# Kernel tuning notes

Hardware: AMD Instinct MI355X
Metric: run time of the kernel (lower is better)

The kernel has to match this reference:

```python
import jax, jax.numpy as jnp
import numpy as np

N_NODES = 500_000
N_EDGES = 16_000_000
F_IN, F_HID, F_OUT = 5, 5, 8


def _gcn_conv(x, W, b, src, dst, norm, n):
    # x: [N, Fin] -> transform first (cheaper than transforming messages)
    h = x @ W                              # [N, Fout]
    msg = h[src] * norm[:, None]           # [E', Fout] gather + per-edge scale
    out = jax.ops.segment_sum(msg, dst, num_segments=n)  # scatter-add over dst
    return out + b


def setup_inputs() -> dict:
    key = jax.random.key(0)
    ks = jax.random.split(key, 6)
    x = jax.random.normal(ks[0], (N_NODES, F_IN), dtype=jnp.float32)
    edge_index = jax.random.randint(ks[1], (2, N_EDGES), 0, N_NODES, dtype=jnp.int32)
    # Glorot-ish init for the two GCNConv layers
    W1 = jax.random.normal(ks[2], (F_IN, F_HID), dtype=jnp.float32) / np.sqrt(F_IN)
    b1 = jnp.zeros((F_HID,), dtype=jnp.float32)
    W2 = jax.random.normal(ks[3], (F_HID, F_OUT), dtype=jnp.float32) / np.sqrt(F_HID)
    b2 = jnp.zeros((F_OUT,), dtype=jnp.float32)
    return {"x": x, "edge_index": edge_index, "W1": W1, "b1": b1, "W2": W2, "b2": b2}


def reference(x, edge_index, W1, b1, W2, b2):
    n = x.shape[0]
    # GCNConv default: add self-loops, symmetric D^-1/2 A D^-1/2 normalization
    loops = jnp.arange(n, dtype=edge_index.dtype)
    src = jnp.concatenate([edge_index[0], loops])
    dst = jnp.concatenate([edge_index[1], loops])
    deg = jax.ops.segment_sum(jnp.ones_like(dst, dtype=x.dtype), dst, num_segments=n)
    dinv = jnp.where(deg > 0, jax.lax.rsqrt(deg), 0.0)
    norm = dinv[src] * dinv[dst]           # [E + N]

    h = _gcn_conv(x, W1, b1, src, dst, norm, n)
    h = jax.nn.relu(h)
    # F.dropout with training=False is the identity (eval-mode reference)
    h = _gcn_conv(h, W2, b2, src, dst, norm, n)
    return jax.nn.log_softmax(h, axis=1)
```

## Files before the change

kernel.cpp:

```cpp
#include <hip/hip_runtime.h>
#include <math.h>


#define FIN 5
#define FHID 5
#define FOUT 8
#define RB 256
#define EPA 24576
#define NBUCK_MAX 2048
#define OCAP 10240

typedef _Float16 half8 __attribute__((ext_vector_type(8)));
typedef int int4v __attribute__((ext_vector_type(4)));


__global__ void k_scan1(const int* __restrict__ t, int* __restrict__ scn,
                        int* __restrict__ partial, int n) {
    __shared__ int sh[256];
    int tx = threadIdx.x;
    int i = blockIdx.x * 256 + tx;
    int v = (i < n) ? t[i] : 0;
    sh[tx] = v;
    __syncthreads();
    for (int off = 1; off < 256; off <<= 1) {
        int add = (tx >= off) ? sh[tx - off] : 0;
        __syncthreads();
        sh[tx] += add;
        __syncthreads();
    }
    if (i < n) scn[i] = sh[tx] - v;
    if (tx == 255) partial[blockIdx.x] = sh[255];
}

__global__ void k_scan2(int* __restrict__ partial, int nb) {
    __shared__ int sh[256];
    __shared__ int carry;
    int tx = threadIdx.x;
    if (tx == 0) carry = 0;
    __syncthreads();
    for (int base = 0; base < nb; base += 256) {
        int i = base + tx;
        int v = (i < nb) ? partial[i] : 0;
        int c0 = carry;
        sh[tx] = v;
        __syncthreads();
        for (int off = 1; off < 256; off <<= 1) {
            int add = (tx >= off) ? sh[tx - off] : 0;
            __syncthreads();
            sh[tx] += add;
            __syncthreads();
        }
        if (i < nb) partial[i] = c0 + sh[tx] - v;
        __syncthreads();
        if (tx == 0) carry = c0 + sh[255];
        __syncthreads();
    }
}


__global__ void k_histA(const int* __restrict__ dst, int* __restrict__ cnt,
                        int e, int nbuck, int nblkA) {
    __shared__ int hist[NBUCK_MAX];
    int tx = threadIdx.x, blk = blockIdx.x;
    for (int b = tx; b < nbuck; b += 1024) hist[b] = 0;
    __syncthreads();
    size_t base = (size_t)blk * EPA;
    const int4v* dst4 = (const int4v*)dst;
    for (int k = 0; k < EPA / 4096; ++k) {
        size_t e4 = base / 4 + (size_t)k * 1024 + tx;
        size_t i = e4 * 4;
        if (i + 3 < (size_t)e) {
            int4v d4 = __builtin_nontemporal_load(&dst4[e4]);
#pragma unroll
            for (int j = 0; j < 4; ++j) atomicAdd(&hist[d4[j] >> 8], 1);
        } else {
            for (int j = 0; j < 4; ++j) {
                size_t ii = i + j;
                if (ii < (size_t)e) atomicAdd(&hist[dst[ii] >> 8], 1);
            }
        }
    }
    __syncthreads();
    for (int b = tx; b < nbuck; b += 1024) cnt[(size_t)b * nblkA + blk] = hist[b];
}

__global__ void k_scatterA(const int* __restrict__ src, const int* __restrict__ dst,
                           const int* __restrict__ scn, const int* __restrict__ part,
                           unsigned int* __restrict__ binnedA,
                           int e, int nbuck, int nblkA) {
    __shared__ int lstart[NBUCK_MAX];
    __shared__ int cur[NBUCK_MAX];
    __shared__ int gbase[NBUCK_MAX];
    __shared__ unsigned int staged[EPA];
    int tx = threadIdx.x, blk = blockIdx.x;
    for (int b = tx; b < NBUCK_MAX; b += 1024) lstart[b] = 0;
    for (int b = tx; b < nbuck; b += 1024) {
        size_t idx = (size_t)b * nblkA + blk;
        gbase[b] = scn[idx] + part[idx >> 8];
    }
    __syncthreads();
    size_t base = (size_t)blk * EPA;
    const int4v* dst4 = (const int4v*)dst;
    const int4v* src4 = (const int4v*)src;
    for (int k = 0; k < EPA / 4096; ++k) {
        size_t e4 = base / 4 + (size_t)k * 1024 + tx;
        size_t i = e4 * 4;
        if (i + 3 < (size_t)e) {
            int4v d4 = dst4[e4];
#pragma unroll
            for (int j = 0; j < 4; ++j) atomicAdd(&lstart[d4[j] >> 8], 1);
        } else {
            for (int j = 0; j < 4; ++j) {
                size_t ii = i + j;
                if (ii < (size_t)e) atomicAdd(&lstart[dst[ii] >> 8], 1);
            }
        }
    }
    __syncthreads();
    int j0 = tx, j1 = tx + 1024;
    int c0 = lstart[j0], c1 = lstart[j1];
    for (int off = 1; off < NBUCK_MAX; off <<= 1) {
        int a0 = (j0 >= off) ? lstart[j0 - off] : 0;
        int a1 = (j1 >= off) ? lstart[j1 - off] : 0;
        __syncthreads();
        lstart[j0] += a0; lstart[j1] += a1;
        __syncthreads();
    }
    int e0 = lstart[j0] - c0, e1 = lstart[j1] - c1;
    __syncthreads();
    lstart[j0] = e0; lstart[j1] = e1;
    cur[j0] = e0;    cur[j1] = e1;
    __syncthreads();
    for (int k = 0; k < EPA / 4096; ++k) {
        size_t e4 = base / 4 + (size_t)k * 1024 + tx;
        size_t i = e4 * 4;
        if (i + 3 < (size_t)e) {
            int4v d4 = dst4[e4];
            int4v s4 = src4[e4];
#pragma unroll
            for (int j = 0; j < 4; ++j) {
                int d = d4[j];
                int pos = atomicAdd(&cur[d >> 8], 1);
                staged[pos] = ((unsigned int)(d & (RB - 1)) << 19) | (unsigned int)s4[j];
            }
        } else {
            for (int j = 0; j < 4; ++j) {
                size_t ii = i + j;
                if (ii < (size_t)e) {
                    int d = dst[ii];
                    int pos = atomicAdd(&cur[d >> 8], 1);
                    staged[pos] = ((unsigned int)(d & (RB - 1)) << 19) | (unsigned int)src[ii];
                }
            }
        }
    }
    __syncthreads();
    int grp = tx >> 4, lane = tx & 15;
    for (int b = grp; b < nbuck; b += 64) {
        int ls = lstart[b];
        int le = (b + 1 < NBUCK_MAX) ? lstart[b + 1] : 0;
        int cnt = le - ls;
        int gb = gbase[b];
        for (int k = lane; k < cnt; k += 16)
            binnedA[gb + k] = staged[ls + k];
    }
}


__global__ void k_passC(const unsigned int* __restrict__ binnedA,
                        const int* __restrict__ scn, const int* __restrict__ part,
                        const float* __restrict__ x,
                        half8* __restrict__ g1, unsigned int* __restrict__ binned3,
                        int* __restrict__ nodeptr,
                        int n, int e, int nbuck, int nblkA) {
    __shared__ int hist[RB];
    __shared__ int scanbuf[RB];
    __shared__ int cur[RB];
    __shared__ unsigned int obuf[OCAP];
    int tx = threadIdx.x, b = blockIdx.x;
    if (tx < RB) hist[tx] = 0;
    __syncthreads();
    size_t i0 = (size_t)b * nblkA;
    int start = scn[i0] + part[i0 >> 8];
    int end;
    if (b + 1 < nbuck) {
        size_t i1 = (size_t)(b + 1) * nblkA;
        end = scn[i1] + part[i1 >> 8];
    } else {
        end = e;
    }
    int len = end - start;
    for (int i = start + tx; i < end; i += 512)
        atomicAdd(&hist[binnedA[i] >> 19], 1);
    __syncthreads();
    int v = 0;
    if (tx < RB) { v = hist[tx]; scanbuf[tx] = v; }
    __syncthreads();
    for (int off = 1; off < RB; off <<= 1) {
        int add = 0;
        if (tx < RB && tx >= off) add = scanbuf[tx - off];
        __syncthreads();
        if (tx < RB) scanbuf[tx] += add;
        __syncthreads();
    }
    if (tx < RB) {
        int excl = scanbuf[tx] - v;
        nodeptr[(size_t)b * RB + tx] = start + excl;
        cur[tx] = excl;
        int node = b * RB + tx;
        if (node < n) {
            float d = rsqrtf((float)(v + 1));
            const float* xp = x + (size_t)node * FIN;
            half8 row = {};
#pragma unroll
            for (int f = 0; f < FIN; ++f) row[f] = (_Float16)(xp[f] * d);
            row[5] = (_Float16)d;
            g1[node] = row;
        }
    }
    if (b == nbuck - 1 && tx == 0) nodeptr[(size_t)nbuck * RB] = end;
    __syncthreads();
    if (len <= OCAP) {
        for (int i = start + tx; i < end; i += 512) {
            unsigned int p = binnedA[i];
            int pos = atomicAdd(&cur[p >> 19], 1);
            obuf[pos] = p & 0x7FFFFu;
        }
        __syncthreads();
        for (int j = tx; j < len; j += 512)
            binned3[start + j] = obuf[j];
    } else {
        for (int i = start + tx; i < end; i += 512) {
            unsigned int p = binnedA[i];
            int pos = atomicAdd(&cur[p >> 19], 1);
            binned3[start + pos] = p & 0x7FFFFu;
        }
    }
}


__global__ void k_vagg1(const unsigned int* __restrict__ ed,
                        const int* __restrict__ nodeptr,
                        const half8* __restrict__ g1,
                        const float* __restrict__ W1, const float* __restrict__ b1,
                        half8* __restrict__ g2, int n) {
    int tid = blockIdx.x * blockDim.x + threadIdx.x;
    int node = tid >> 4;
    int lane = tid & 15;
    if (node >= n) return;
    int o0 = nodeptr[node];
    int o1 = nodeptr[node + 1];
    float a0 = 0, a1 = 0, a2 = 0, a3 = 0, a4 = 0;
    for (int k = o0 + lane; k < o1; k += 16) {
        unsigned int s = __builtin_nontemporal_load(&ed[k]);
        half8 hv = g1[s];
        a0 += (float)hv[0]; a1 += (float)hv[1]; a2 += (float)hv[2];
        a3 += (float)hv[3]; a4 += (float)hv[4];
    }
#pragma unroll
    for (int off = 1; off < 16; off <<= 1) {
        a0 += __shfl_xor(a0, off, 16);
        a1 += __shfl_xor(a1, off, 16);
        a2 += __shfl_xor(a2, off, 16);
        a3 += __shfl_xor(a3, off, 16);
        a4 += __shfl_xor(a4, off, 16);
    }
    if (lane == 0) {
        half8 gi = g1[node];
        float d = (float)gi[5];
        float v[FIN];
        v[0] = (a0 + (float)gi[0]) * d;
        v[1] = (a1 + (float)gi[1]) * d;
        v[2] = (a2 + (float)gi[2]) * d;
        v[3] = (a3 + (float)gi[3]) * d;
        v[4] = (a4 + (float)gi[4]) * d;
        half8 go = {};
#pragma unroll
        for (int j = 0; j < FHID; ++j) {
            float s = b1[j];
#pragma unroll
            for (int k = 0; k < FIN; ++k) s = fmaf(v[k], W1[k * FHID + j], s);
            go[j] = (_Float16)(fmaxf(s, 0.0f) * d);
        }
        go[5] = gi[5];
        g2[node] = go;
    }
}

__global__ void k_vagg2(const unsigned int* __restrict__ ed,
                        const int* __restrict__ nodeptr,
                        const half8* __restrict__ g2,
                        const float* __restrict__ W2, const float* __restrict__ b2,
                        float* __restrict__ out, int n) {
    int tid = blockIdx.x * blockDim.x + threadIdx.x;
    int node = tid >> 4;
    int lane = tid & 15;
    if (node >= n) return;
    int o0 = nodeptr[node];
    int o1 = nodeptr[node + 1];
    float a0 = 0, a1 = 0, a2 = 0, a3 = 0, a4 = 0;
    for (int k = o0 + lane; k < o1; k += 16) {
        unsigned int s = __builtin_nontemporal_load(&ed[k]);
        half8 hv = g2[s];
        a0 += (float)hv[0]; a1 += (float)hv[1]; a2 += (float)hv[2];
        a3 += (float)hv[3]; a4 += (float)hv[4];
    }
#pragma unroll
    for (int off = 1; off < 16; off <<= 1) {
        a0 += __shfl_xor(a0, off, 16);
        a1 += __shfl_xor(a1, off, 16);
        a2 += __shfl_xor(a2, off, 16);
        a3 += __shfl_xor(a3, off, 16);
        a4 += __shfl_xor(a4, off, 16);
    }
    if (lane == 0) {
        half8 gi = g2[node];
        float d = (float)gi[5];
        float v[FHID];
        v[0] = (a0 + (float)gi[0]) * d;
        v[1] = (a1 + (float)gi[1]) * d;
        v[2] = (a2 + (float)gi[2]) * d;
        v[3] = (a3 + (float)gi[3]) * d;
        v[4] = (a4 + (float)gi[4]) * d;
        float o[FOUT];
        float m = -1e30f;
#pragma unroll
        for (int j = 0; j < FOUT; ++j) {
            float s = b2[j];
#pragma unroll
            for (int k = 0; k < FHID; ++k) s = fmaf(v[k], W2[k * FOUT + j], s);
            o[j] = s;
            m = fmaxf(m, s);
        }
        float ssum = 0.0f;
#pragma unroll
        for (int j = 0; j < FOUT; ++j) ssum += expf(o[j] - m);
        float lse = m + logf(ssum);
        float* op = out + (size_t)node * FOUT;
#pragma unroll
        for (int j = 0; j < FOUT; ++j) op[j] = o[j] - lse;
    }
}


__global__ void f_init_deg(float* __restrict__ deg, int n) {
    int i = blockIdx.x * blockDim.x + threadIdx.x;
    if (i < n) deg[i] = 1.0f;
}
__global__ void f_count_deg(const int* __restrict__ dst, float* __restrict__ deg, int e) {
    int i = blockIdx.x * blockDim.x + threadIdx.x;
    if (i < e) atomicAdd(&deg[dst[i]], 1.0f);
}
__global__ void f_finish_deg_g1(const float* __restrict__ x, float* __restrict__ dinv,
                                float* __restrict__ g1, int n) {
    int i = blockIdx.x * blockDim.x + threadIdx.x;
    if (i >= n) return;
    float d = rsqrtf(dinv[i]);
    dinv[i] = d;
#pragma unroll
    for (int f = 0; f < FIN; ++f) g1[(size_t)i * FIN + f] = x[(size_t)i * FIN + f] * d;
}
__global__ void f_scatter5(const int* __restrict__ src, const int* __restrict__ dst,
                           const float* __restrict__ g, float* __restrict__ acc, int e) {
    int i = blockIdx.x * blockDim.x + threadIdx.x;
    if (i >= e) return;
    int s = src[i], d = dst[i];
    float* a = acc + (size_t)d * 5;
    const float* gp = g + (size_t)s * 5;
    atomicAdd(a + 0, gp[0]);
    atomicAdd(a + 1, gp[1]);
    atomicAdd(a + 2, gp[2]);
    atomicAdd(a + 3, gp[3]);
    atomicAdd(a + 4, gp[4]);
}
__global__ void f_update1(const float* __restrict__ dinv, float* __restrict__ g,
                          float* __restrict__ acc, const float* __restrict__ W1,
                          const float* __restrict__ b1, int n) {
    int i = blockIdx.x * blockDim.x + threadIdx.x;
    if (i >= n) return;
    float d = dinv[i];
    float v[FIN];
#pragma unroll
    for (int f = 0; f < FIN; ++f) {
        size_t idx = (size_t)i * FIN + f;
        v[f] = (acc[idx] + g[idx]) * d;
        acc[idx] = 0.0f;
    }
#pragma unroll
    for (int j = 0; j < FHID; ++j) {
        float s = b1[j];
#pragma unroll
        for (int k = 0; k < FIN; ++k) s += v[k] * W1[k * FHID + j];
        g[(size_t)i * FHID + j] = fmaxf(s, 0.0f) * d;
    }
}
__global__ void f_update2(const float* __restrict__ dinv, const float* __restrict__ g,
                          const float* __restrict__ acc, const float* __restrict__ W2,
                          const float* __restrict__ b2, float* __restrict__ out, int n) {
    int i = blockIdx.x * blockDim.x + threadIdx.x;
    if (i >= n) return;
    float d = dinv[i];
    float v[FHID];
#pragma unroll
    for (int f = 0; f < FHID; ++f) v[f] = (acc[(size_t)i * FHID + f] + g[(size_t)i * FHID + f]) * d;
    float o[FOUT];
    float m = -1e30f;
#pragma unroll
    for (int j = 0; j < FOUT; ++j) {
        float s = b2[j];
#pragma unroll
        for (int k = 0; k < FHID; ++k) s += v[k] * W2[k * FOUT + j];
        o[j] = s;
        m = fmaxf(m, s);
    }
    float ssum = 0.0f;
#pragma unroll
    for (int j = 0; j < FOUT; ++j) ssum += expf(o[j] - m);
    float lse = m + logf(ssum);
#pragma unroll
    for (int j = 0; j < FOUT; ++j) out[(size_t)i * FOUT + j] = o[j] - lse;
}


extern "C" void kernel_launch(void* const* d_in, const int* in_sizes, int n_in,
                              void* d_out, int out_size, void* d_ws, size_t ws_size,
                              hipStream_t stream) {
    const float* x  = (const float*)d_in[0];
    const int*   ei = (const int*)d_in[1];
    const float* W1 = (const float*)d_in[2];
    const float* b1 = (const float*)d_in[3];
    const float* W2 = (const float*)d_in[4];
    const float* b2 = (const float*)d_in[5];

    const int n = in_sizes[0] / FIN;
    const int e = in_sizes[1] / 2;
    const int* src = ei;
    const int* dst = ei + e;

    const int nbuck = (n + RB - 1) / RB;
    const int nblkA = (e + EPA - 1) / EPA;
    const size_t m = (size_t)nbuck * nblkA;
    const int nsb = (int)((m + 255) / 256);

    size_t off = 0;
    auto al = [&](size_t bytes) { size_t o = off; off = (off + bytes + 15) & ~(size_t)15; return o; };
    int*          cnt     = (int*)((char*)d_ws + al(m * 4));
    int*          scn     = (int*)((char*)d_ws + al(m * 4));
    int*          part    = (int*)((char*)d_ws + al((size_t)nsb * 4));
    int*          nptr    = (int*)((char*)d_ws + al(((size_t)nbuck * RB + 1) * 4));
    half8*        g1      = (half8*)((char*)d_ws + al((size_t)n * 16));
    unsigned int* binnedA = (unsigned int*)((char*)d_ws + al((size_t)e * 4));
    unsigned int* binned3 = (unsigned int*)((char*)d_ws + al((size_t)e * 4));
    half8*        g2      = (half8*)binnedA;
    const size_t need = off;

    if (ws_size >= need && n <= 524288 && n >= 1 && (e & 3) == 0 && nbuck <= NBUCK_MAX) {
        k_histA<<<nblkA, 1024, 0, stream>>>(dst, cnt, e, nbuck, nblkA);
        k_scan1<<<nsb, 256, 0, stream>>>(cnt, scn, part, (int)m);
        k_scan2<<<1, 256, 0, stream>>>(part, nsb);
        k_scatterA<<<nblkA, 1024, 0, stream>>>(src, dst, scn, part, binnedA, e, nbuck, nblkA);
        k_passC<<<nbuck, 512, 0, stream>>>(binnedA, scn, part, x, g1, binned3, nptr, n, e, nbuck, nblkA);
        const int ga = (int)(((size_t)n * 16 + 511) / 512);
        k_vagg1<<<ga, 512, 0, stream>>>(binned3, nptr, g1, W1, b1, g2, n);
        k_vagg2<<<ga, 512, 0, stream>>>(binned3, nptr, g2, W2, b2, (float*)d_out, n);
        return;
    }

    const int B = 256;
    const int gn = (n + B - 1) / B;
    const int ge = (e + B - 1) / B;
    float* fdinv = (float*)d_ws;
    float* fg    = fdinv + n;
    float* facc  = fg + (size_t)5 * n;
    hipMemsetAsync(facc, 0, (size_t)5 * n * sizeof(float), stream);
    f_init_deg<<<gn, B, 0, stream>>>(fdinv, n);
    f_count_deg<<<ge, B, 0, stream>>>(dst, fdinv, e);
    f_finish_deg_g1<<<gn, B, 0, stream>>>(x, fdinv, fg, n);
    f_scatter5<<<ge, B, 0, stream>>>(src, dst, fg, facc, e);
    f_update1<<<gn, B, 0, stream>>>(fdinv, fg, facc, W1, b1, n);
    f_scatter5<<<ge, B, 0, stream>>>(src, dst, fg, facc, e);
    f_update2<<<gn, B, 0, stream>>>(fdinv, fg, facc, W2, b2, (float*)d_out, n);
}
```

Measured before the change: 509.6 us.

## Split aggregation by source-node half to shrink gather working set

Each destination's edge list is now partitioned into sources below and above n/2, with a midptr array marking the split. Each layer's aggregation becomes two passes: the first gathers from the low half of the feature table into fp32 partial accumulators, and the second gathers from the high half and finishes the layer. The goal is to keep each pass's random-gather working set small enough to stay cache-resident, at the cost of extra kernel launches and partial-sum traffic. Separately, scatterA reuses the per-block histogram from histA instead of recomputing it, and reads src/dst with nontemporal loads.

```diff
diff --git a/kernel.cpp b/kernel.cpp
--- a/kernel.cpp
+++ b/kernel.cpp
@@ -12,6 +12,7 @@
 
 typedef _Float16 half8 __attribute__((ext_vector_type(8)));
 typedef int int4v __attribute__((ext_vector_type(4)));
+typedef float fl4 __attribute__((ext_vector_type(4)));
 
 
 __global__ void k_scan1(const int* __restrict__ t, int* __restrict__ scn,
@@ -85,6 +86,7 @@
 }
 
 __global__ void k_scatterA(const int* __restrict__ src, const int* __restrict__ dst,
+                           const int* __restrict__ cnt,
                            const int* __restrict__ scn, const int* __restrict__ part,
                            unsigned int* __restrict__ binnedA,
                            int e, int nbuck, int nblkA) {
@@ -93,11 +95,29 @@
     __shared__ int gbase[NBUCK_MAX];
     __shared__ unsigned int staged[EPA];
     int tx = threadIdx.x, blk = blockIdx.x;
-    for (int b = tx; b < NBUCK_MAX; b += 1024) lstart[b] = 0;
-    for (int b = tx; b < nbuck; b += 1024) {
-        size_t idx = (size_t)b * nblkA + blk;
-        gbase[b] = scn[idx] + part[idx >> 8];
-    }
+    for (int b = tx; b < NBUCK_MAX; b += 1024) {
+        if (b < nbuck) {
+            size_t idx = (size_t)b * nblkA + blk;
+            lstart[b] = cnt[idx];
+            gbase[b] = scn[idx] + part[idx >> 8];
+        } else {
+            lstart[b] = 0;
+        }
+    }
+    __syncthreads();
+    int j0 = tx, j1 = tx + 1024;
+    int c0 = lstart[j0], c1 = lstart[j1];
+    for (int off = 1; off < NBUCK_MAX; off <<= 1) {
+        int a0 = (j0 >= off) ? lstart[j0 - off] : 0;
+        int a1 = (j1 >= off) ? lstart[j1 - off] : 0;
+        __syncthreads();
+        lstart[j0] += a0; lstart[j1] += a1;
+        __syncthreads();
+    }
+    int e0 = lstart[j0] - c0, e1 = lstart[j1] - c1;
+    __syncthreads();
+    lstart[j0] = e0; lstart[j1] = e1;
+    cur[j0] = e0;    cur[j1] = e1;
     __syncthreads();
     size_t base = (size_t)blk * EPA;
     const int4v* dst4 = (const int4v*)dst;
@@ -106,37 +126,8 @@
         size_t e4 = base / 4 + (size_t)k * 1024 + tx;
         size_t i = e4 * 4;
         if (i + 3 < (size_t)e) {
-            int4v d4 = dst4[e4];
-#pragma unroll
-            for (int j = 0; j < 4; ++j) atomicAdd(&lstart[d4[j] >> 8], 1);
-        } else {
-            for (int j = 0; j < 4; ++j) {
-                size_t ii = i + j;
-                if (ii < (size_t)e) atomicAdd(&lstart[dst[ii] >> 8], 1);
-            }
-        }
-    }
-    __syncthreads();
-    int j0 = tx, j1 = tx + 1024;
-    int c0 = lstart[j0], c1 = lstart[j1];
-    for (int off = 1; off < NBUCK_MAX; off <<= 1) {
-        int a0 = (j0 >= off) ? lstart[j0 - off] : 0;
-        int a1 = (j1 >= off) ? lstart[j1 - off] : 0;
-        __syncthreads();
-        lstart[j0] += a0; lstart[j1] += a1;
-        __syncthreads();
-    }
-    int e0 = lstart[j0] - c0, e1 = lstart[j1] - c1;
-    __syncthreads();
-    lstart[j0] = e0; lstart[j1] = e1;
-    cur[j0] = e0;    cur[j1] = e1;
-    __syncthreads();
-    for (int k = 0; k < EPA / 4096; ++k) {
-        size_t e4 = base / 4 + (size_t)k * 1024 + tx;
-        size_t i = e4 * 4;
-        if (i + 3 < (size_t)e) {
-            int4v d4 = dst4[e4];
-            int4v s4 = src4[e4];
+            int4v d4 = __builtin_nontemporal_load(&dst4[e4]);
+            int4v s4 = __builtin_nontemporal_load(&src4[e4]);
 #pragma unroll
             for (int j = 0; j < 4; ++j) {
                 int d = d4[j];
@@ -159,9 +150,9 @@
     for (int b = grp; b < nbuck; b += 64) {
         int ls = lstart[b];
         int le = (b + 1 < NBUCK_MAX) ? lstart[b + 1] : 0;
-        int cnt = le - ls;
+        int len = le - ls;
         int gb = gbase[b];
-        for (int k = lane; k < cnt; k += 16)
+        for (int k = lane; k < len; k += 16)
             binnedA[gb + k] = staged[ls + k];
     }
 }
@@ -171,14 +162,14 @@
                         const int* __restrict__ scn, const int* __restrict__ part,
                         const float* __restrict__ x,
                         half8* __restrict__ g1, unsigned int* __restrict__ binned3,
-                        int* __restrict__ nodeptr,
-                        int n, int e, int nbuck, int nblkA) {
-    __shared__ int hist[RB];
-    __shared__ int scanbuf[RB];
-    __shared__ int cur[RB];
+                        int* __restrict__ nodeptr, int* __restrict__ midptr,
+                        int n, int e, int nbuck, int nblkA, unsigned int half) {
+    __shared__ int hist[2 * RB];
+    __shared__ int scanbuf[2 * RB];
+    __shared__ int cur[2 * RB];
     __shared__ unsigned int obuf[OCAP];
     int tx = threadIdx.x, b = blockIdx.x;
-    if (tx < RB) hist[tx] = 0;
+    hist[tx] = 0;
     __syncthreads();
     size_t i0 = (size_t)b * nblkA;
     int start = scn[i0] + part[i0 >> 8];
@@ -190,26 +181,30 @@
         end = e;
     }
     int len = end - start;
-    for (int i = start + tx; i < end; i += 512)
-        atomicAdd(&hist[binnedA[i] >> 19], 1);
-    __syncthreads();
-    int v = 0;
-    if (tx < RB) { v = hist[tx]; scanbuf[tx] = v; }
-    __syncthreads();
-    for (int off = 1; off < RB; off <<= 1) {
-        int add = 0;
-        if (tx < RB && tx >= off) add = scanbuf[tx - off];
-        __syncthreads();
-        if (tx < RB) scanbuf[tx] += add;
-        __syncthreads();
-    }
+    for (int i = start + tx; i < end; i += 512) {
+        unsigned int p = binnedA[i];
+        int key = (int)((p >> 19) << 1) | ((p & 0x7FFFFu) >= half ? 1 : 0);
+        atomicAdd(&hist[key], 1);
+    }
+    __syncthreads();
+    int v = hist[tx];
+    scanbuf[tx] = v;
+    __syncthreads();
+    for (int off = 1; off < 2 * RB; off <<= 1) {
+        int add = (tx >= off) ? scanbuf[tx - off] : 0;
+        __syncthreads();
+        scanbuf[tx] += add;
+        __syncthreads();
+    }
+    int excl = scanbuf[tx] - v;
+    cur[tx] = excl;
+    if ((tx & 1) == 0) nodeptr[(size_t)b * RB + (tx >> 1)] = start + excl;
+    else               midptr[(size_t)b * RB + (tx >> 1)]  = start + excl;
     if (tx < RB) {
-        int excl = scanbuf[tx] - v;
-        nodeptr[(size_t)b * RB + tx] = start + excl;
-        cur[tx] = excl;
         int node = b * RB + tx;
         if (node < n) {
-            float d = rsqrtf((float)(v + 1));
+            int deg = hist[2 * tx] + hist[2 * tx + 1];
+            float d = rsqrtf((float)(deg + 1));
             const float* xp = x + (size_t)node * FIN;
             half8 row = {};
 #pragma unroll
@@ -223,7 +218,8 @@
     if (len <= OCAP) {
         for (int i = start + tx; i < end; i += 512) {
             unsigned int p = binnedA[i];
-            int pos = atomicAdd(&cur[p >> 19], 1);
+            int key = (int)((p >> 19) << 1) | ((p & 0x7FFFFu) >= half ? 1 : 0);
+            int pos = atomicAdd(&cur[key], 1);
             obuf[pos] = p & 0x7FFFFu;
         }
         __syncthreads();
@@ -232,28 +228,28 @@
     } else {
         for (int i = start + tx; i < end; i += 512) {
             unsigned int p = binnedA[i];
-            int pos = atomicAdd(&cur[p >> 19], 1);
+            int key = (int)((p >> 19) << 1) | ((p & 0x7FFFFu) >= half ? 1 : 0);
+            int pos = atomicAdd(&cur[key], 1);
             binned3[start + pos] = p & 0x7FFFFu;
         }
     }
 }
 
 
-__global__ void k_vagg1(const unsigned int* __restrict__ ed,
-                        const int* __restrict__ nodeptr,
-                        const half8* __restrict__ g1,
-                        const float* __restrict__ W1, const float* __restrict__ b1,
-                        half8* __restrict__ g2, int n) {
+__global__ void k_vphase0(const unsigned int* __restrict__ ed,
+                          const int* __restrict__ nodeptr, const int* __restrict__ midptr,
+                          const half8* __restrict__ g,
+                          fl4* __restrict__ acc4, float* __restrict__ acc1, int n) {
     int tid = blockIdx.x * blockDim.x + threadIdx.x;
     int node = tid >> 4;
     int lane = tid & 15;
     if (node >= n) return;
     int o0 = nodeptr[node];
-    int o1 = nodeptr[node + 1];
+    int om = midptr[node];
     float a0 = 0, a1 = 0, a2 = 0, a3 = 0, a4 = 0;
-    for (int k = o0 + lane; k < o1; k += 16) {
+    for (int k = o0 + lane; k < om; k += 16) {
         unsigned int s = __builtin_nontemporal_load(&ed[k]);
-        half8 hv = g1[s];
+        half8 hv = g[s];
         a0 += (float)hv[0]; a1 += (float)hv[1]; a2 += (float)hv[2];
         a3 += (float)hv[3]; a4 += (float)hv[4];
     }
@@ -266,42 +262,28 @@
         a4 += __shfl_xor(a4, off, 16);
     }
     if (lane == 0) {
-        half8 gi = g1[node];
-        float d = (float)gi[5];
-        float v[FIN];
-        v[0] = (a0 + (float)gi[0]) * d;
-        v[1] = (a1 + (float)gi[1]) * d;
-        v[2] = (a2 + (float)gi[2]) * d;
-        v[3] = (a3 + (float)gi[3]) * d;
-        v[4] = (a4 + (float)gi[4]) * d;
-        half8 go = {};
-#pragma unroll
-        for (int j = 0; j < FHID; ++j) {
-            float s = b1[j];
-#pragma unroll
-            for (int k = 0; k < FIN; ++k) s = fmaf(v[k], W1[k * FHID + j], s);
-            go[j] = (_Float16)(fmaxf(s, 0.0f) * d);
-        }
-        go[5] = gi[5];
-        g2[node] = go;
-    }
-}
-
-__global__ void k_vagg2(const unsigned int* __restrict__ ed,
-                        const int* __restrict__ nodeptr,
-                        const half8* __restrict__ g2,
-                        const float* __restrict__ W2, const float* __restrict__ b2,
-                        float* __restrict__ out, int n) {
+        fl4 p; p.x = a0; p.y = a1; p.z = a2; p.w = a3;
+        __builtin_nontemporal_store(p, &acc4[node]);
+        __builtin_nontemporal_store(a4, &acc1[node]);
+    }
+}
+
+__global__ void k_vp1_l1(const unsigned int* __restrict__ ed,
+                         const int* __restrict__ nodeptr, const int* __restrict__ midptr,
+                         const half8* __restrict__ g1,
+                         const fl4* __restrict__ acc4, const float* __restrict__ acc1,
+                         const float* __restrict__ W1, const float* __restrict__ b1,
+                         half8* __restrict__ g2, int n) {
     int tid = blockIdx.x * blockDim.x + threadIdx.x;
     int node = tid >> 4;
     int lane = tid & 15;
     if (node >= n) return;
-    int o0 = nodeptr[node];
+    int om = midptr[node];
     int o1 = nodeptr[node + 1];
     float a0 = 0, a1 = 0, a2 = 0, a3 = 0, a4 = 0;
-    for (int k = o0 + lane; k < o1; k += 16) {
+    for (int k = om + lane; k < o1; k += 16) {
         unsigned int s = __builtin_nontemporal_load(&ed[k]);
-        half8 hv = g2[s];
+        half8 hv = g1[s];
         a0 += (float)hv[0]; a1 += (float)hv[1]; a2 += (float)hv[2];
         a3 += (float)hv[3]; a4 += (float)hv[4];
     }
@@ -314,14 +296,67 @@
         a4 += __shfl_xor(a4, off, 16);
     }
     if (lane == 0) {
+        fl4 pp = acc4[node];
+        float p4 = acc1[node];
+        half8 gi = g1[node];
+        float d = (float)gi[5];
+        float v[FIN];
+        v[0] = (a0 + pp.x + (float)gi[0]) * d;
+        v[1] = (a1 + pp.y + (float)gi[1]) * d;
+        v[2] = (a2 + pp.z + (float)gi[2]) * d;
+        v[3] = (a3 + pp.w + (float)gi[3]) * d;
+        v[4] = (a4 + p4   + (float)gi[4]) * d;
+        half8 go = {};
+#pragma unroll
+        for (int j = 0; j < FHID; ++j) {
+            float s = b1[j];
+#pragma unroll
+            for (int k = 0; k < FIN; ++k) s = fmaf(v[k], W1[k * FHID + j], s);
+            go[j] = (_Float16)(fmaxf(s, 0.0f) * d);
+        }
+        go[5] = gi[5];
+        g2[node] = go;
+    }
+}
+
+__global__ void k_vp1_l2(const unsigned int* __restrict__ ed,
+                         const int* __restrict__ nodeptr, const int* __restrict__ midptr,
+                         const half8* __restrict__ g2,
+                         const fl4* __restrict__ acc4, const float* __restrict__ acc1,
+                         const float* __restrict__ W2, const float* __restrict__ b2,
+                         float* __restrict__ out, int n) {
+    int tid = blockIdx.x * blockDim.x + threadIdx.x;
+    int node = tid >> 4;
+    int lane = tid & 15;
+    if (node >= n) return;
+    int om = midptr[node];
+    int o1 = nodeptr[node + 1];
+    float a0 = 0, a1 = 0, a2 = 0, a3 = 0, a4 = 0;
+    for (int k = om + lane; k < o1; k += 16) {
+        unsigned int s = __builtin_nontemporal_load(&ed[k]);
+        half8 hv = g2[s];
+        a0 += (float)hv[0]; a1 += (float)hv[1]; a2 += (float)hv[2];
+        a3 += (float)hv[3]; a4 += (float)hv[4];
+    }
+#pragma unroll
+    for (int off = 1; off < 16; off <<= 1) {
+        a0 += __shfl_xor(a0, off, 16);
+        a1 += __shfl_xor(a1, off, 16);
+        a2 += __shfl_xor(a2, off, 16);
+        a3 += __shfl_xor(a3, off, 16);
+        a4 += __shfl_xor(a4, off, 16);
+    }
+    if (lane == 0) {
+        fl4 pp = acc4[node];
+        float p4 = acc1[node];
         half8 gi = g2[node];
         float d = (float)gi[5];
         float v[FHID];
-        v[0] = (a0 + (float)gi[0]) * d;
-        v[1] = (a1 + (float)gi[1]) * d;
-        v[2] = (a2 + (float)gi[2]) * d;
-        v[3] = (a3 + (float)gi[3]) * d;
-        v[4] = (a4 + (float)gi[4]) * d;
+        v[0] = (a0 + pp.x + (float)gi[0]) * d;
+        v[1] = (a1 + pp.y + (float)gi[1]) * d;
+        v[2] = (a2 + pp.z + (float)gi[2]) * d;
+        v[3] = (a3 + pp.w + (float)gi[3]) * d;
+        v[4] = (a4 + p4   + (float)gi[4]) * d;
         float o[FOUT];
         float m = -1e30f;
 #pragma unroll
@@ -448,21 +483,29 @@
     int*          scn     = (int*)((char*)d_ws + al(m * 4));
     int*          part    = (int*)((char*)d_ws + al((size_t)nsb * 4));
     int*          nptr    = (int*)((char*)d_ws + al(((size_t)nbuck * RB + 1) * 4));
+    int*          mptr    = (int*)((char*)d_ws + al((size_t)nbuck * RB * 4));
     half8*        g1      = (half8*)((char*)d_ws + al((size_t)n * 16));
     unsigned int* binnedA = (unsigned int*)((char*)d_ws + al((size_t)e * 4));
     unsigned int* binned3 = (unsigned int*)((char*)d_ws + al((size_t)e * 4));
     half8*        g2      = (half8*)binnedA;
+    fl4*          acc4    = (fl4*)((char*)binnedA + (size_t)16 * 1024 * 1024);
+    float*        acc1    = (float*)((char*)binnedA + (size_t)32 * 1024 * 1024);
     const size_t need = off;
 
-    if (ws_size >= need && n <= 524288 && n >= 1 && (e & 3) == 0 && nbuck <= NBUCK_MAX) {
+    if (ws_size >= need && n <= 524288 && n >= 1 && (e & 3) == 0 && nbuck <= NBUCK_MAX &&
+        (size_t)e * 4 >= (size_t)34 * 1024 * 1024 && (size_t)n * 16 <= (size_t)16 * 1024 * 1024) {
+        const unsigned int half = (unsigned int)(n >> 1);
         k_histA<<<nblkA, 1024, 0, stream>>>(dst, cnt, e, nbuck, nblkA);
         k_scan1<<<nsb, 256, 0, stream>>>(cnt, scn, part, (int)m);
         k_scan2<<<1, 256, 0, stream>>>(part, nsb);
-        k_scatterA<<<nblkA, 1024, 0, stream>>>(src, dst, scn, part, binnedA, e, nbuck, nblkA);
-        k_passC<<<nbuck, 512, 0, stream>>>(binnedA, scn, part, x, g1, binned3, nptr, n, e, nbuck, nblkA);
+        k_scatterA<<<nblkA, 1024, 0, stream>>>(src, dst, cnt, scn, part, binnedA, e, nbuck, nblkA);
+        k_passC<<<nbuck, 512, 0, stream>>>(binnedA, scn, part, x, g1, binned3, nptr, mptr,
+                                           n, e, nbuck, nblkA, half);
         const int ga = (int)(((size_t)n * 16 + 511) / 512);
-        k_vagg1<<<ga, 512, 0, stream>>>(binned3, nptr, g1, W1, b1, g2, n);
-        k_vagg2<<<ga, 512, 0, stream>>>(binned3, nptr, g2, W2, b2, (float*)d_out, n);
+        k_vphase0<<<ga, 512, 0, stream>>>(binned3, nptr, mptr, g1, acc4, acc1, n);
+        k_vp1_l1<<<ga, 512, 0, stream>>>(binned3, nptr, mptr, g1, acc4, acc1, W1, b1, g2, n);
+        k_vphase0<<<ga, 512, 0, stream>>>(binned3, nptr, mptr, g2, acc4, acc1, n);
+        k_vp1_l2<<<ga, 512, 0, stream>>>(binned3, nptr, mptr, g2, acc4, acc1, W2, b2, (float*)d_out, n);
         return;
     }
 
```

Result: faster. 489.8 us (-3.9%).
